# Kernel optimization log

Measured on AMD Instinct MI355X. Metric: run time of the kernel, lower is better.

The kernel has to match this reference:

```python
import jax, jax.numpy as jnp
from jax import lax
import numpy as np

KERNEL = 3
PAD = KERNEL // 2


def _normalized_weights(affinity):
    # affinity: [B, 8, H, W] -> 9-tap weights [B, 9, H, W] with center at index 4
    aff_sum = jnp.sum(jnp.abs(affinity), axis=1, keepdims=True)
    aff_norm = affinity / aff_sum
    center = 1.0 - jnp.sum(aff_norm, axis=1, keepdims=True)
    # Original loop uses affinity channels 0..3 for taps before center, 4..7 after
    return jnp.concatenate([aff_norm[:, :4], center, aff_norm[:, 4:]], axis=1)


def setup_inputs() -> dict:
    key = jax.random.key(0)
    k1, k2 = jax.random.split(key)
    B, H, W = 8, 480, 640
    affinity = jax.random.normal(k1, (B, KERNEL * KERNEL - 1, H, W), dtype=jnp.float32)
    feature = jax.random.normal(k2, (B, 1, H, W), dtype=jnp.float32)
    return {"affinity": affinity, "feature": feature, "times": 24}


def reference(affinity, feature, times):
    weights = _normalized_weights(affinity)  # [B, 9, H, W]
    B, C, H, W = feature.shape

    def step(f, _):
        fp = jnp.pad(f, ((0, 0), (0, 0), (PAD, PAD), (PAD, PAD)))
        # 9 shifted views stacked on a tap axis: [B, 9, C, H, W]
        shifts = jnp.stack(
            [fp[:, :, i:i + H, j:j + W] for i in range(KERNEL) for j in range(KERNEL)],
            axis=1,
        )
        f_new = jnp.sum(shifts * weights[:, :, None, :, :], axis=1)
        return f_new, None

    out, _ = lax.scan(step, feature, None, length=times)
    return out
```

## Files before the change

kernel.cpp:

```cpp
#include <hip/hip_runtime.h>
#include <hip/hip_fp16.h>
#include <cstddef>


#define HIMG 480
#define WIMG 640
#define HW   (HIMG * WIMG)
#define BN   8

#define TILE   40
#define TSTEPS 12
#define IH     13
#define WHL    12
#define SW     66
#define PITCH  68
#define NT     512

#define WS_FRAME_B  ((size_t)BN * HW * 4)
#define WS_WA_B     ((size_t)BN * HW * 16)
#define WS_WC_B     ((size_t)BN * HW * 4)
#define WS_NEED     (WS_FRAME_B + WS_WA_B + WS_WC_B)

template <int MODE>
__global__ __launch_bounds__(NT, 4) void affprop12(
    const float* __restrict__ aff,
    __half2* __restrict__ wA,
    float* __restrict__ wC,
    const float* __restrict__ src,
    float* __restrict__ dst)
{
    __shared__ float fA[SW * PITCH];
    __shared__ float fB[SW * PITCH];

    const int tid = threadIdx.x;
    const int ox  = blockIdx.x * TILE;
    const int oy  = blockIdx.y * TILE;
    const int b   = blockIdx.z;

    const float* __restrict__ sb = src + (size_t)b * HW;
    float*       __restrict__ db = dst + (size_t)b * HW;

    for (int i = tid; i < SW * SW; i += NT) {
        int r  = i / SW;
        int c  = i - r * SW;
        int gy = oy - IH + r;
        int gx = ox - IH + c;
        float v = 0.f;
        if ((unsigned)gy < (unsigned)HIMG && (unsigned)gx < (unsigned)WIMG)
            v = sb[gy * WIMG + gx];
        fA[r * PITCH + c] = v;
    }
    for (int i = tid; i < SW * PITCH / 4; i += NT)
        *(float4*)&fB[4 * i] = make_float4(0.f, 0.f, 0.f, 0.f);

    const int c  = tid & 63;
    const int g  = tid >> 6;
    const int sc = c + 1;

    __half2 wv[8][4];
    float   wcc[8];

    #pragma unroll
    for (int i = 0; i < 8; ++i) {
        const int gy = oy - WHL + 8 * g + i;
        const int gx = ox - WHL + c;
        const bool in = (unsigned)gy < (unsigned)HIMG && (unsigned)gx < (unsigned)WIMG;
        const size_t idx = (size_t)b * HW + (size_t)gy * WIMG + gx;

        if (MODE == 1) {
            if (in) {
                union { float4 f4; __half2 h[4]; } u;
                u.f4 = *(const float4*)(wA + 4 * idx);
                wv[i][0] = u.h[0]; wv[i][1] = u.h[1];
                wv[i][2] = u.h[2]; wv[i][3] = u.h[3];
                wcc[i] = wC[idx];
            } else {
                __half2 z = __floats2half2_rn(0.f, 0.f);
                wv[i][0] = z; wv[i][1] = z; wv[i][2] = z; wv[i][3] = z;
                wcc[i] = 0.f;
            }
        } else {
            float w[8];
            float s = 0.f;
            if (in) {
                const float* ap = aff + (size_t)b * 8 * HW + (size_t)gy * WIMG + gx;
                #pragma unroll
                for (int k = 0; k < 8; ++k) { w[k] = ap[(size_t)k * HW]; s += fabsf(w[k]); }
            } else {
                #pragma unroll
                for (int k = 0; k < 8; ++k) w[k] = 0.f;
                s = 1.f;
            }
            float rr  = in ? 1.0f / s : 0.f;
            float acc = 0.f;
            #pragma unroll
            for (int k = 0; k < 8; ++k) { w[k] *= rr; acc += w[k]; }

            union { float4 f4; __half2 h[4]; } u;
            u.h[0] = __floats2half2_rn(w[0], w[1]);
            u.h[1] = __floats2half2_rn(w[2], w[3]);
            u.h[2] = __floats2half2_rn(w[4], w[5]);
            u.h[3] = __floats2half2_rn(w[6], w[7]);
            wv[i][0] = u.h[0]; wv[i][1] = u.h[1];
            wv[i][2] = u.h[2]; wv[i][3] = u.h[3];
            wcc[i] = in ? 1.0f - acc : 0.f;

            if (MODE == 0) {
                if ((unsigned)(gy - oy) < (unsigned)TILE &&
                    (unsigned)(gx - ox) < (unsigned)TILE) {
                    *(float4*)(wA + 4 * idx) = u.f4;
                    wC[idx] = wcc[i];
                }
            }
        }
    }
    __syncthreads();

    const float* fin = fA;
    float*       fo  = fB;

    #pragma unroll 1
    for (int s = 0; s < TSTEPS; ++s) {
        const float* rp = fin + (8 * g) * PITCH + c;
        float a0 = rp[0], a1 = rp[1], a2 = rp[2];
        rp += PITCH;
        float b0 = rp[0], b1 = rp[1], b2 = rp[2];
        float* wp = fo + (8 * g + 1) * PITCH + sc;

        #pragma unroll
        for (int i = 0; i < 8; ++i) {
            rp += PITCH;
            float c0 = rp[0], c1 = rp[1], c2 = rp[2];

            float o = wcc[i] * b1
                + __low2float (wv[i][0]) * a0
                + __high2float(wv[i][0]) * a1
                + __low2float (wv[i][1]) * a2
                + __high2float(wv[i][1]) * b0
                + __low2float (wv[i][2]) * b2
                + __high2float(wv[i][2]) * c0
                + __low2float (wv[i][3]) * c1
                + __high2float(wv[i][3]) * c2;

            *wp = o;
            wp += PITCH;
            a0 = b0; a1 = b1; a2 = b2;
            b0 = c0; b1 = c1; b2 = c2;
        }
        __syncthreads();
        const float* t = fin; fin = fo; fo = (float*)t;
    }

    for (int i = tid; i < TILE * (TILE / 4); i += NT) {
        int r  = i / (TILE / 4);
        int c4 = (i - r * (TILE / 4)) * 4;
        const float* p = fin + (IH + r) * PITCH + IH + c4;
        float4 v = make_float4(p[0], p[1], p[2], p[3]);
        *(float4*)&db[(size_t)(oy + r) * WIMG + ox + c4] = v;
    }
}

extern "C" void kernel_launch(void* const* d_in, const int* in_sizes, int n_in,
                              void* d_out, int out_size, void* d_ws, size_t ws_size,
                              hipStream_t stream)
{
    const float* aff  = (const float*)d_in[0];
    const float* feat = (const float*)d_in[1];
    float* out = (float*)d_out;

    char* ws = (char*)d_ws;
    float*   wsFrame = (float*)ws;
    __half2* wA      = (__half2*)(ws + WS_FRAME_B);
    float*   wC      = (float*)(ws + WS_FRAME_B + WS_WA_B);

    dim3 blk(NT, 1, 1);
    dim3 grd(WIMG / TILE, HIMG / TILE, BN);

    if (ws_size >= WS_NEED) {
        affprop12<0><<<grd, blk, 0, stream>>>(aff, wA, wC, feat, wsFrame);
        affprop12<1><<<grd, blk, 0, stream>>>(aff, wA, wC, wsFrame, out);
    } else {
        affprop12<2><<<grd, blk, 0, stream>>>(aff, nullptr, nullptr, feat, wsFrame);
        affprop12<2><<<grd, blk, 0, stream>>>(aff, nullptr, nullptr, wsFrame, out);
    }
}
```

Before: 219.9 us.

## Remap threads to 1x8 row strips with register-resident state and drop weight cache

Each thread now owns a horizontal strip of 8 pixels in one row, not a vertical column of 8, and keeps its current values in registers across steps. Per step it reads only the top and bottom rows plus two side pixels from LDS. The shared pitch becomes 77 to reduce bank conflicts for the new access pattern. The precomputed-weight workspace path is removed, so both launches recompute normalized weights from the affinity input, which adds global reads in the second pass. The final output is written with scalar strided stores instead of float4 stores.

Measured after the change: 356.6 us. +62.2%, slower.

```diff
diff --git a/kernel.cpp b/kernel.cpp
--- a/kernel.cpp
+++ b/kernel.cpp
@@ -12,25 +12,17 @@
 #define TSTEPS 12
 #define IH     13
 #define WHL    12
-#define SW     66
-#define PITCH  68
+#define SWD    66
+#define PITCH  77
 #define NT     512
 
-#define WS_FRAME_B  ((size_t)BN * HW * 4)
-#define WS_WA_B     ((size_t)BN * HW * 16)
-#define WS_WC_B     ((size_t)BN * HW * 4)
-#define WS_NEED     (WS_FRAME_B + WS_WA_B + WS_WC_B)
-
-template <int MODE>
 __global__ __launch_bounds__(NT, 4) void affprop12(
     const float* __restrict__ aff,
-    __half2* __restrict__ wA,
-    float* __restrict__ wC,
     const float* __restrict__ src,
     float* __restrict__ dst)
 {
-    __shared__ float fA[SW * PITCH];
-    __shared__ float fB[SW * PITCH];
+    __shared__ float fA[SWD * PITCH];
+    __shared__ float fB[SWD * PITCH];
 
     const int tid = threadIdx.x;
     const int ox  = blockIdx.x * TILE;
@@ -40,9 +32,9 @@
     const float* __restrict__ sb = src + (size_t)b * HW;
     float*       __restrict__ db = dst + (size_t)b * HW;
 
-    for (int i = tid; i < SW * SW; i += NT) {
-        int r  = i / SW;
-        int c  = i - r * SW;
+    for (int i = tid; i < SWD * SWD; i += NT) {
+        int r  = i / SWD;
+        int c  = i - r * SWD;
         int gy = oy - IH + r;
         int gx = ox - IH + c;
         float v = 0.f;
@@ -50,36 +42,21 @@
             v = sb[gy * WIMG + gx];
         fA[r * PITCH + c] = v;
     }
-    for (int i = tid; i < SW * PITCH / 4; i += NT)
-        *(float4*)&fB[4 * i] = make_float4(0.f, 0.f, 0.f, 0.f);
+    for (int i = tid; i < SWD * PITCH; i += NT)
+        fB[i] = 0.f;
 
-    const int c  = tid & 63;
-    const int g  = tid >> 6;
-    const int sc = c + 1;
+    const int u = tid & 7;
+    const int r = tid >> 3;
 
     __half2 wv[8][4];
     float   wcc[8];
-
-    #pragma unroll
-    for (int i = 0; i < 8; ++i) {
-        const int gy = oy - WHL + 8 * g + i;
-        const int gx = ox - WHL + c;
-        const bool in = (unsigned)gy < (unsigned)HIMG && (unsigned)gx < (unsigned)WIMG;
-        const size_t idx = (size_t)b * HW + (size_t)gy * WIMG + gx;
-
-        if (MODE == 1) {
-            if (in) {
-                union { float4 f4; __half2 h[4]; } u;
-                u.f4 = *(const float4*)(wA + 4 * idx);
-                wv[i][0] = u.h[0]; wv[i][1] = u.h[1];
-                wv[i][2] = u.h[2]; wv[i][3] = u.h[3];
-                wcc[i] = wC[idx];
-            } else {
-                __half2 z = __floats2half2_rn(0.f, 0.f);
-                wv[i][0] = z; wv[i][1] = z; wv[i][2] = z; wv[i][3] = z;
-                wcc[i] = 0.f;
-            }
-        } else {
+    {
+        const int gy = oy - WHL + r;
+        const bool rin = (unsigned)gy < (unsigned)HIMG;
+        #pragma unroll
+        for (int j = 0; j < 8; ++j) {
+            const int gx = ox - WHL + 8 * u + j;
+            const bool in = rin && (unsigned)gx < (unsigned)WIMG;
             float w[8];
             float s = 0.f;
             if (in) {
@@ -95,68 +72,75 @@
             float acc = 0.f;
             #pragma unroll
             for (int k = 0; k < 8; ++k) { w[k] *= rr; acc += w[k]; }
-
-            union { float4 f4; __half2 h[4]; } u;
-            u.h[0] = __floats2half2_rn(w[0], w[1]);
-            u.h[1] = __floats2half2_rn(w[2], w[3]);
-            u.h[2] = __floats2half2_rn(w[4], w[5]);
-            u.h[3] = __floats2half2_rn(w[6], w[7]);
-            wv[i][0] = u.h[0]; wv[i][1] = u.h[1];
-            wv[i][2] = u.h[2]; wv[i][3] = u.h[3];
-            wcc[i] = in ? 1.0f - acc : 0.f;
-
-            if (MODE == 0) {
-                if ((unsigned)(gy - oy) < (unsigned)TILE &&
-                    (unsigned)(gx - ox) < (unsigned)TILE) {
-                    *(float4*)(wA + 4 * idx) = u.f4;
-                    wC[idx] = wcc[i];
-                }
-            }
+            wv[j][0] = __floats2half2_rn(w[0], w[1]);
+            wv[j][1] = __floats2half2_rn(w[2], w[3]);
+            wv[j][2] = __floats2half2_rn(w[4], w[5]);
+            wv[j][3] = __floats2half2_rn(w[6], w[7]);
+            wcc[j] = in ? 1.0f - acc : 0.f;
         }
     }
     __syncthreads();
+
+    const int tbase = r * PITCH + 8 * u;
+    const int mbase = tbase + PITCH;
+    const int bbase = mbase + PITCH;
+
+    float v[8];
+    #pragma unroll
+    for (int j = 0; j < 8; ++j) v[j] = fA[mbase + 1 + j];
 
     const float* fin = fA;
     float*       fo  = fB;
 
     #pragma unroll 1
     for (int s = 0; s < TSTEPS; ++s) {
-        const float* rp = fin + (8 * g) * PITCH + c;
-        float a0 = rp[0], a1 = rp[1], a2 = rp[2];
-        rp += PITCH;
-        float b0 = rp[0], b1 = rp[1], b2 = rp[2];
-        float* wp = fo + (8 * g + 1) * PITCH + sc;
+        float T[10], B[10];
+        #pragma unroll
+        for (int k = 0; k < 10; ++k) T[k] = fin[tbase + k];
+        #pragma unroll
+        for (int k = 0; k < 10; ++k) B[k] = fin[bbase + k];
+        float M0 = fin[mbase];
+        float M9 = fin[mbase + 9];
+
+        float M[10];
+        M[0] = M0;
+        #pragma unroll
+        for (int j = 0; j < 8; ++j) M[j + 1] = v[j];
+        M[9] = M9;
+
+        float nv[8];
+        #pragma unroll
+        for (int j = 0; j < 8; ++j) {
+            nv[j] = wcc[j] * M[j + 1]
+                + __low2float (wv[j][0]) * T[j]
+                + __high2float(wv[j][0]) * T[j + 1]
+                + __low2float (wv[j][1]) * T[j + 2]
+                + __high2float(wv[j][1]) * M[j]
+                + __low2float (wv[j][2]) * M[j + 2]
+                + __high2float(wv[j][2]) * B[j]
+                + __low2float (wv[j][3]) * B[j + 1]
+                + __high2float(wv[j][3]) * B[j + 2];
+        }
 
         #pragma unroll
-        for (int i = 0; i < 8; ++i) {
-            rp += PITCH;
-            float c0 = rp[0], c1 = rp[1], c2 = rp[2];
+        for (int j = 0; j < 8; ++j) v[j] = nv[j];
 
-            float o = wcc[i] * b1
-                + __low2float (wv[i][0]) * a0
-                + __high2float(wv[i][0]) * a1
-                + __low2float (wv[i][1]) * a2
-                + __high2float(wv[i][1]) * b0
-                + __low2float (wv[i][2]) * b2
-                + __high2float(wv[i][2]) * c0
-                + __low2float (wv[i][3]) * c1
-                + __high2float(wv[i][3]) * c2;
-
-            *wp = o;
-            wp += PITCH;
-            a0 = b0; a1 = b1; a2 = b2;
-            b0 = c0; b1 = c1; b2 = c2;
+        if (s < TSTEPS - 1) {
+            #pragma unroll
+            for (int j = 0; j < 8; ++j) fo[mbase + 1 + j] = nv[j];
+            __syncthreads();
+            const float* t = fin; fin = fo; fo = (float*)t;
         }
-        __syncthreads();
-        const float* t = fin; fin = fo; fo = (float*)t;
     }
 
-    for (int i = tid; i < TILE * (TILE / 4); i += NT) {
-        int r  = i / (TILE / 4);
-        int c4 = (i - r * (TILE / 4)) * 4;
-        const float* p = fin + (IH + r) * PITCH + IH + c4;
-        float4 v = make_float4(p[0], p[1], p[2], p[3]);
-        *(float4*)&db[(size_t)(oy + r) * WIMG + ox + c4] = v;
+    if ((unsigned)(r - WHL) < (unsigned)TILE) {
+        const int gy = oy + (r - WHL);
+        #pragma unroll
+        for (int j = 0; j < 8; ++j) {
+            const int wcol = 8 * u + j;
+            if ((unsigned)(wcol - WHL) < (unsigned)TILE)
+                db[(size_t)gy * WIMG + ox + (wcol - WHL)] = v[j];
+        }
     }
 }
 
@@ -167,20 +151,11 @@
     const float* aff  = (const float*)d_in[0];
     const float* feat = (const float*)d_in[1];
     float* out = (float*)d_out;
-
-    char* ws = (char*)d_ws;
-    float*   wsFrame = (float*)ws;
-    __half2* wA      = (__half2*)(ws + WS_FRAME_B);
-    float*   wC      = (float*)(ws + WS_FRAME_B + WS_WA_B);
+    float* ws  = (float*)d_ws;
 
     dim3 blk(NT, 1, 1);
     dim3 grd(WIMG / TILE, HIMG / TILE, BN);
 
-    if (ws_size >= WS_NEED) {
-        affprop12<0><<<grd, blk, 0, stream>>>(aff, wA, wC, feat, wsFrame);
-        affprop12<1><<<grd, blk, 0, stream>>>(aff, wA, wC, wsFrame, out);
-    } else {
-        affprop12<2><<<grd, blk, 0, stream>>>(aff, nullptr, nullptr, feat, wsFrame);
-        affprop12<2><<<grd, blk, 0, stream>>>(aff, nullptr, nullptr, wsFrame, out);
-    }
+    affprop12<<<grd, blk, 0, stream>>>(aff, feat, ws);
+    affprop12<<<grd, blk, 0, stream>>>(aff, ws, out);
 }
```
